# Kernel optimization log

Hardware: AMD Instinct MI355X
Metric: run time of the kernel (lower is better)

## Reference

```python
import jax, jax.numpy as jnp
import numpy as np

DOWNSAMPLE = 1  # downsample_factor


def _grid(out_h, out_w):
    # rows: x in [-1,1] along width, y in [-1,1] along height, ones
    x_t = jnp.linspace(-1.0, 1.0, out_w, dtype=jnp.float32)
    y_t = jnp.linspace(-1.0, 1.0, out_h, dtype=jnp.float32)
    xg = jnp.tile(x_t[None, :], (out_h, 1)).reshape(-1)
    yg = jnp.tile(y_t[:, None], (1, out_w)).reshape(-1)
    return jnp.stack([xg, yg, jnp.ones_like(xg)], axis=0)  # [3, P]


def spatial_transform(X, theta):
    B, C, H, W = X.shape
    out_h, out_w = H // DOWNSAMPLE, W // DOWNSAMPLE
    grid = _grid(out_h, out_w)                               # [3, P]
    Tg = jnp.einsum('bij,jp->bip', theta.reshape(B, 2, 3), grid)  # [B,2,P]
    x_s, y_s = Tg[:, 0], Tg[:, 1]                            # [B, P]

    # map from [-1,1] to pixel coords (same convention as original)
    x = (x_s + 1.0) * (W / 2.0)
    y = (y_s + 1.0) * (H / 2.0)
    x0 = jnp.floor(x).astype(jnp.int32)
    x1 = x0 + 1
    y0 = jnp.floor(y).astype(jnp.int32)
    y1 = y0 + 1
    x0c = jnp.clip(x0, 0, W - 1)
    x1c = jnp.clip(x1, 0, W - 1)
    y0c = jnp.clip(y0, 0, H - 1)
    y1c = jnp.clip(y1, 0, H - 1)

    im = jnp.transpose(X, (0, 2, 3, 1)).reshape(B, H * W, C)  # [B, HW, C]

    def gather(yi, xi):
        idx = yi * W + xi                                      # [B, P]
        return jnp.take_along_axis(im, idx[:, :, None], axis=1)  # [B, P, C]

    Ia = gather(y0c, x0c)
    Ib = gather(y1c, x0c)
    Ic = gather(y0c, x1c)
    Id = gather(y1c, x1c)

    x0f = x0c.astype(jnp.float32)
    x1f = x1c.astype(jnp.float32)
    y0f = y0c.astype(jnp.float32)
    y1f = y1c.astype(jnp.float32)
    wa = ((x1f - x) * (y1f - y))[:, :, None]
    wb = ((x1f - x) * (y - y0f))[:, :, None]
    wc = ((x - x0f) * (y1f - y))[:, :, None]
    wd = ((x - x0f) * (y - y0f))[:, :, None]

    out = wa * Ia + wb * Ib + wc * Ic + wd * Id               # [B, P, C]
    out = out.reshape(B, out_h, out_w, C)
    return jnp.transpose(out, (0, 3, 1, 2))                   # NCHW


def setup_inputs() -> dict:
    key = jax.random.key(0)
    kx, kt = jax.random.split(key)
    X = jax.random.normal(kx, (32, 3, 512, 512), dtype=jnp.float32)
    # theta near identity + noise for sensible transforms
    ident = jnp.array([1.0, 0.0, 0.0, 0.0, 1.0, 0.0], dtype=jnp.float32)
    theta = ident[None, :] + 0.1 * jax.random.normal(kt, (32, 6), dtype=jnp.float32)
    return {"X": X, "theta": theta}


def reference(X, theta):
    return spatial_transform(X, theta)
```

## Files before the change

### kernel.cpp

```cpp
#include <hip/hip_runtime.h>


#define ST_H 512
#define ST_W 512
#define ST_C 3

typedef float f2 __attribute__((ext_vector_type(2)));
struct __attribute__((packed, aligned(4))) f2_a4 { f2 v; };

__global__ __launch_bounds__(256) void st_bilinear_kernel(
    const float* __restrict__ X,
    const float* __restrict__ theta,
    float* __restrict__ out,
    int B, int chunk)
{
    int bid = blockIdx.x;
    bid = (bid & 7) * chunk + (bid >> 3);

    const int gid = bid * 256 + threadIdx.x;
    const int pix = gid & (ST_H * ST_W - 1);
    const int b   = gid >> 18;
    if (b >= B) return;

    const int h = pix >> 9;
    const int w = pix & 511;

    const float* t = theta + b * 6;
    const float t00 = t[0], t01 = t[1], t02 = t[2];
    const float t10 = t[3], t11 = t[4], t12 = t[5];

    const float xg = (float)(-1.0 + (2.0 / 511.0) * (double)w);
    const float yg = (float)(-1.0 + (2.0 / 511.0) * (double)h);

    const float x_s = t00 * xg + t01 * yg + t02;
    const float y_s = t10 * xg + t11 * yg + t12;
    const float x = (x_s + 1.0f) * (0.5f * ST_W);
    const float y = (y_s + 1.0f) * (0.5f * ST_H);

    const int x0 = (int)floorf(x);
    const int y0 = (int)floorf(y);
    const int x1 = x0 + 1, y1 = y0 + 1;

    const int x0c = min(max(x0, 0), ST_W - 1);
    const int x1c = min(max(x1, 0), ST_W - 1);
    const int y0c = min(max(y0, 0), ST_H - 1);
    const int y1c = min(max(y1, 0), ST_H - 1);

    const float x0f = (float)x0c, x1f = (float)x1c;
    const float y0f = (float)y0c, y1f = (float)y1c;
    const float wa = (x1f - x) * (y1f - y);
    const float wb = (x1f - x) * (y - y0f);
    const float wc = (x - x0f) * (y1f - y);
    const float wd = (x - x0f) * (y - y0f);

    const int xa = min(max(x0, 0), ST_W - 2);
    const bool hi = (x0 >= ST_W - 1);
    const bool lo = (x0 < 0);

    const int ia = y0c * ST_W + xa;
    const int ib = y1c * ST_W + xa;

    const float* __restrict__ Xb = X + (size_t)b * (ST_C * ST_H * ST_W);
    float* __restrict__ ob = out + (size_t)b * (ST_C * ST_H * ST_W) + pix;

#pragma unroll
    for (int c = 0; c < ST_C; ++c) {
        const float* __restrict__ Xc = Xb + c * (ST_H * ST_W);
        const f2 v0 = ((const f2_a4*)(Xc + ia))->v;
        const f2 v1 = ((const f2_a4*)(Xc + ib))->v;
        const float Ia = hi ? v0.y : v0.x;
        const float Ic = lo ? v0.x : v0.y;
        const float Ib = hi ? v1.y : v1.x;
        const float Id = lo ? v1.x : v1.y;
        const float v = wa * Ia + wb * Ib + wc * Ic + wd * Id;
        __builtin_nontemporal_store(v, ob + c * (ST_H * ST_W));
    }
}

extern "C" void kernel_launch(void* const* d_in, const int* in_sizes, int n_in,
                              void* d_out, int out_size, void* d_ws, size_t ws_size,
                              hipStream_t stream) {
    const float* X     = (const float*)d_in[0];
    const float* theta = (const float*)d_in[1];
    float* out         = (float*)d_out;

    const int B = in_sizes[1] / 6;
    const int total = B * ST_H * ST_W;
    const int block = 256;
    const int grid = (total + block - 1) / block;
    const int chunk = grid / 8;

    st_bilinear_kernel<<<grid, block, 0, stream>>>(X, theta, out, B, chunk);
}
```

Before: 47.45 us.

## Compute two adjacent output pixels per thread sharing one four-wide gather

```diff
diff --git a/kernel.cpp b/kernel.cpp
--- a/kernel.cpp
+++ b/kernel.cpp
@@ -4,9 +4,25 @@
 #define ST_H 512
 #define ST_W 512
 #define ST_C 3
+#define ST_HW (ST_H * ST_W)
 
 typedef float f2 __attribute__((ext_vector_type(2)));
+typedef float f4 __attribute__((ext_vector_type(4)));
 struct __attribute__((packed, aligned(4))) f2_a4 { f2 v; };
+struct __attribute__((packed, aligned(4))) f4_a4 { f4 v; };
+
+__device__ __forceinline__ float pick3(f4 v, int o) {
+    float r = v.x;
+    r = (o == 1) ? v.y : r;
+    r = (o == 2) ? v.z : r;
+    return r;
+}
+__device__ __forceinline__ float pick3h(f4 v, int o) {
+    float r = v.y;
+    r = (o == 1) ? v.z : r;
+    r = (o == 2) ? v.w : r;
+    return r;
+}
 
 __global__ __launch_bounds__(256) void st_bilinear_kernel(
     const float* __restrict__ X,
@@ -17,64 +33,95 @@
     int bid = blockIdx.x;
     bid = (bid & 7) * chunk + (bid >> 3);
 
-    const int gid = bid * 256 + threadIdx.x;
-    const int pix = gid & (ST_H * ST_W - 1);
-    const int b   = gid >> 18;
-    if (b >= B) return;
-
-    const int h = pix >> 9;
-    const int w = pix & 511;
+    const int h  = bid & (ST_H - 1);
+    const int b  = bid >> 9;
+    const int w0 = (int)threadIdx.x * 2;
 
     const float* t = theta + b * 6;
     const float t00 = t[0], t01 = t[1], t02 = t[2];
     const float t10 = t[3], t11 = t[4], t12 = t[5];
 
-    const float xg = (float)(-1.0 + (2.0 / 511.0) * (double)w);
-    const float yg = (float)(-1.0 + (2.0 / 511.0) * (double)h);
+    const float STEP = (float)(2.0 / 511.0);
+    const float yg = fmaf((float)h, STEP, -1.0f);
+    const float cx = fmaf(t01, yg, t02);
+    const float cy = fmaf(t11, yg, t12);
 
-    const float x_s = t00 * xg + t01 * yg + t02;
-    const float y_s = t10 * xg + t11 * yg + t12;
-    const float x = (x_s + 1.0f) * (0.5f * ST_W);
-    const float y = (y_s + 1.0f) * (0.5f * ST_H);
+    float wa[2], wbm[2], wcm[2], wdm[2];
+    int xa[2], ta[2], tb[2];
+    bool hi[2], lo[2];
 
-    const int x0 = (int)floorf(x);
-    const int y0 = (int)floorf(y);
-    const int x1 = x0 + 1, y1 = y0 + 1;
+#pragma unroll
+    for (int j = 0; j < 2; ++j) {
+        const float xg = fmaf((float)(w0 + j), STEP, -1.0f);
+        const float x = (fmaf(t00, xg, cx) + 1.0f) * 256.0f;
+        const float y = (fmaf(t10, xg, cy) + 1.0f) * 256.0f;
+        const int x0 = (int)floorf(x);
+        const int y0 = (int)floorf(y);
+        const int x0c = min(max(x0, 0), ST_W - 1);
+        const int x1c = min(max(x0 + 1, 0), ST_W - 1);
+        const int y0c = min(max(y0, 0), ST_H - 1);
+        const int y1c = min(max(y0 + 1, 0), ST_H - 1);
+        const float x0f = (float)x0c, x1f = (float)x1c;
+        const float y0f = (float)y0c, y1f = (float)y1c;
+        wa[j]  = (x1f - x) * (y1f - y);
+        wbm[j] = (x1f - x) * (y - y0f);
+        wcm[j] = (x - x0f) * (y1f - y);
+        wdm[j] = (x - x0f) * (y - y0f);
+        xa[j] = min(max(x0, 0), ST_W - 2);
+        ta[j] = y0c;
+        tb[j] = y1c;
+        hi[j] = (x0 >= ST_W - 1);
+        lo[j] = (x0 < 0);
+    }
 
-    const int x0c = min(max(x0, 0), ST_W - 1);
-    const int x1c = min(max(x1, 0), ST_W - 1);
-    const int y0c = min(max(y0, 0), ST_H - 1);
-    const int y1c = min(max(y1, 0), ST_H - 1);
+    const int  base = min(xa[0], ST_W - 4);
+    const bool g0 = (xa[0] <= ST_W - 4);
+    const int  o1 = xa[1] - base;
+    const bool g1 = ((unsigned)o1 <= 2u) && (ta[1] == ta[0]) && (tb[1] == tb[0]);
 
-    const float x0f = (float)x0c, x1f = (float)x1c;
-    const float y0f = (float)y0c, y1f = (float)y1c;
-    const float wa = (x1f - x) * (y1f - y);
-    const float wb = (x1f - x) * (y - y0f);
-    const float wc = (x - x0f) * (y1f - y);
-    const float wd = (x - x0f) * (y - y0f);
-
-    const int xa = min(max(x0, 0), ST_W - 2);
-    const bool hi = (x0 >= ST_W - 1);
-    const bool lo = (x0 < 0);
-
-    const int ia = y0c * ST_W + xa;
-    const int ib = y1c * ST_W + xa;
-
-    const float* __restrict__ Xb = X + (size_t)b * (ST_C * ST_H * ST_W);
-    float* __restrict__ ob = out + (size_t)b * (ST_C * ST_H * ST_W) + pix;
+    const float* __restrict__ Xb = X + (size_t)b * (ST_C * ST_HW);
+    float* __restrict__ ob = out + (size_t)b * (ST_C * ST_HW) + h * ST_W + w0;
 
 #pragma unroll
     for (int c = 0; c < ST_C; ++c) {
-        const float* __restrict__ Xc = Xb + c * (ST_H * ST_W);
-        const f2 v0 = ((const f2_a4*)(Xc + ia))->v;
-        const f2 v1 = ((const f2_a4*)(Xc + ib))->v;
-        const float Ia = hi ? v0.y : v0.x;
-        const float Ic = lo ? v0.x : v0.y;
-        const float Ib = hi ? v1.y : v1.x;
-        const float Id = lo ? v1.x : v1.y;
-        const float v = wa * Ia + wb * Ib + wc * Ic + wd * Id;
-        __builtin_nontemporal_store(v, ob + c * (ST_H * ST_W));
+        const float* __restrict__ Xc = Xb + c * ST_HW;
+        const f4 va = ((const f4_a4*)(Xc + ta[0] * ST_W + base))->v;
+        const f4 vb = ((const f4_a4*)(Xc + tb[0] * ST_W + base))->v;
+
+        float pA0, pC0, pB0, pD0;
+        if (g0) {
+            pA0 = va.x; pC0 = va.y; pB0 = vb.x; pD0 = vb.y;
+        } else {
+            const f2 p = ((const f2_a4*)(Xc + ta[0] * ST_W + xa[0]))->v;
+            const f2 q = ((const f2_a4*)(Xc + tb[0] * ST_W + xa[0]))->v;
+            pA0 = p.x; pC0 = p.y; pB0 = q.x; pD0 = q.y;
+        }
+
+        float pA1, pC1, pB1, pD1;
+        if (g1) {
+            pA1 = pick3 (va, o1); pC1 = pick3h(va, o1);
+            pB1 = pick3 (vb, o1); pD1 = pick3h(vb, o1);
+        } else {
+            const f2 p = ((const f2_a4*)(Xc + ta[1] * ST_W + xa[1]))->v;
+            const f2 q = ((const f2_a4*)(Xc + tb[1] * ST_W + xa[1]))->v;
+            pA1 = p.x; pC1 = p.y; pB1 = q.x; pD1 = q.y;
+        }
+
+        const float Ia0 = hi[0] ? pC0 : pA0;
+        const float Ic0 = lo[0] ? pA0 : pC0;
+        const float Ib0 = hi[0] ? pD0 : pB0;
+        const float Id0 = lo[0] ? pB0 : pD0;
+        const float Ia1 = hi[1] ? pC1 : pA1;
+        const float Ic1 = lo[1] ? pA1 : pC1;
+        const float Ib1 = hi[1] ? pD1 : pB1;
+        const float Id1 = lo[1] ? pB1 : pD1;
+
+        f2 v;
+        v.x = wa[0] * Ia0 + wbm[0] * Ib0 + wcm[0] * Ic0 + wdm[0] * Id0;
+        v.y = wa[1] * Ia1 + wbm[1] * Ib1 + wcm[1] * Ic1 + wdm[1] * Id1;
+        __builtin_nontemporal_store(v, (f2*)(ob + c * ST_HW));
     }
+    (void)B;
 }
 
 extern "C" void kernel_launch(void* const* d_in, const int* in_sizes, int n_in,
@@ -85,9 +132,8 @@
     float* out         = (float*)d_out;
 
     const int B = in_sizes[1] / 6;
-    const int total = B * ST_H * ST_W;
     const int block = 256;
-    const int grid = (total + block - 1) / block;
+    const int grid = B * ST_H;
     const int chunk = grid / 8;
 
     st_bilinear_kernel<<<grid, block, 0, stream>>>(X, theta, out, B, chunk);
```

After: 49.45 us. 1.04x slower.

## Stage source footprint per 32x32 output tile in LDS for bilinear sampling

Applied to the files above, without the earlier changes.

```diff
diff --git a/kernel.cpp b/kernel.cpp
--- a/kernel.cpp
+++ b/kernel.cpp
@@ -4,76 +4,154 @@
 #define ST_H 512
 #define ST_W 512
 #define ST_C 3
+#define ST_HW (ST_H * ST_W)
+#define TILE 32
+#define RMAX 48
+#define CPITCH 49
 
 typedef float f2 __attribute__((ext_vector_type(2)));
+typedef float f4 __attribute__((ext_vector_type(4)));
 struct __attribute__((packed, aligned(4))) f2_a4 { f2 v; };
 
-__global__ __launch_bounds__(256) void st_bilinear_kernel(
+__global__ __launch_bounds__(256) void st_bilinear_tiled(
     const float* __restrict__ X,
     const float* __restrict__ theta,
     float* __restrict__ out,
-    int B, int chunk)
+    int chunk)
 {
+    __shared__ float sb[ST_C][RMAX][CPITCH];
+
     int bid = blockIdx.x;
     bid = (bid & 7) * chunk + (bid >> 3);
 
-    const int gid = bid * 256 + threadIdx.x;
-    const int pix = gid & (ST_H * ST_W - 1);
-    const int b   = gid >> 18;
-    if (b >= B) return;
-
-    const int h = pix >> 9;
-    const int w = pix & 511;
+    const int b    = bid >> 8;
+    const int tile = bid & 255;
+    const int h0 = (tile >> 4) << 5;
+    const int w0 = (tile & 15) << 5;
 
     const float* t = theta + b * 6;
     const float t00 = t[0], t01 = t[1], t02 = t[2];
     const float t10 = t[3], t11 = t[4], t12 = t[5];
+    const float STEP = (float)(2.0 / 511.0);
 
-    const float xg = (float)(-1.0 + (2.0 / 511.0) * (double)w);
-    const float yg = (float)(-1.0 + (2.0 / 511.0) * (double)h);
+    float xminf = 1e30f, xmaxf = -1e30f, yminf = 1e30f, ymaxf = -1e30f;
+    {
+        const float xs0 = fmaf((float)w0, STEP, -1.0f);
+        const float xs1 = fmaf((float)(w0 + TILE - 1), STEP, -1.0f);
+        const float ys0 = fmaf((float)h0, STEP, -1.0f);
+        const float ys1 = fmaf((float)(h0 + TILE - 1), STEP, -1.0f);
+        const float xsv[2] = { xs0, xs1 };
+        const float ysv[2] = { ys0, ys1 };
+#pragma unroll
+        for (int i = 0; i < 2; ++i)
+#pragma unroll
+            for (int j = 0; j < 2; ++j) {
+                const float cxc = fmaf(t01, ysv[j], t02);
+                const float cyc = fmaf(t11, ysv[j], t12);
+                const float xx = (fmaf(t00, xsv[i], cxc) + 1.0f) * 256.0f;
+                const float yy = (fmaf(t10, xsv[i], cyc) + 1.0f) * 256.0f;
+                xminf = fminf(xminf, xx); xmaxf = fmaxf(xmaxf, xx);
+                yminf = fminf(yminf, yy); ymaxf = fmaxf(ymaxf, yy);
+            }
+    }
+    const int xlo = (int)floorf(xminf) - 1;
+    const int ylo = (int)floorf(yminf) - 1;
+    const int RX  = (int)floorf(xmaxf) + 2 - xlo + 1;
+    const int RY  = (int)floorf(ymaxf) + 2 - ylo + 1;
 
-    const float x_s = t00 * xg + t01 * yg + t02;
-    const float y_s = t10 * xg + t11 * yg + t12;
-    const float x = (x_s + 1.0f) * (0.5f * ST_W);
-    const float y = (y_s + 1.0f) * (0.5f * ST_H);
+    const int tid  = threadIdx.x;
+    const int trow = tid >> 3;
+    const int tcol = (tid & 7) << 2;
+    const int h = h0 + trow;
 
-    const int x0 = (int)floorf(x);
-    const int y0 = (int)floorf(y);
-    const int x1 = x0 + 1, y1 = y0 + 1;
+    const float yg = fmaf((float)h, STEP, -1.0f);
+    const float cx = fmaf(t01, yg, t02);
+    const float cy = fmaf(t11, yg, t12);
 
-    const int x0c = min(max(x0, 0), ST_W - 1);
-    const int x1c = min(max(x1, 0), ST_W - 1);
-    const int y0c = min(max(y0, 0), ST_H - 1);
-    const int y1c = min(max(y1, 0), ST_H - 1);
+    const float* __restrict__ Xb = X + (size_t)b * (ST_C * ST_HW);
+    float* __restrict__ ob = out + (size_t)b * (ST_C * ST_HW) + h * ST_W + (w0 + tcol);
 
-    const float x0f = (float)x0c, x1f = (float)x1c;
-    const float y0f = (float)y0c, y1f = (float)y1c;
-    const float wa = (x1f - x) * (y1f - y);
-    const float wb = (x1f - x) * (y - y0f);
-    const float wc = (x - x0f) * (y1f - y);
-    const float wd = (x - x0f) * (y - y0f);
+    float acc[ST_C][4];
 
-    const int xa = min(max(x0, 0), ST_W - 2);
-    const bool hi = (x0 >= ST_W - 1);
-    const bool lo = (x0 < 0);
+    if (RX <= CPITCH && RY <= RMAX) {
+        const int lane = tid & 63, wid = tid >> 6;
+        const int colc = min(max(xlo + lane, 0), ST_W - 1);
+#pragma unroll
+        for (int c = 0; c < ST_C; ++c) {
+            const float* __restrict__ Xc = Xb + c * ST_HW;
+            for (int r = wid; r < RY; r += 4) {
+                const int rowc = min(max(ylo + r, 0), ST_H - 1);
+                if (lane < CPITCH)
+                    sb[c][r][lane] = Xc[rowc * ST_W + colc];
+            }
+        }
+        __syncthreads();
 
-    const int ia = y0c * ST_W + xa;
-    const int ib = y1c * ST_W + xa;
+#pragma unroll
+        for (int j = 0; j < 4; ++j) {
+            const float xg = fmaf((float)(w0 + tcol + j), STEP, -1.0f);
+            const float x = (fmaf(t00, xg, cx) + 1.0f) * 256.0f;
+            const float y = (fmaf(t10, xg, cy) + 1.0f) * 256.0f;
+            const int x0 = (int)floorf(x);
+            const int y0 = (int)floorf(y);
+            const int x0c = min(max(x0, 0), ST_W - 1);
+            const int x1c = min(max(x0 + 1, 0), ST_W - 1);
+            const int y0c = min(max(y0, 0), ST_H - 1);
+            const int y1c = min(max(y0 + 1, 0), ST_H - 1);
+            const float wa = ((float)x1c - x) * ((float)y1c - y);
+            const float wb = ((float)x1c - x) * (y - (float)y0c);
+            const float wc = (x - (float)x0c) * ((float)y1c - y);
+            const float wd = (x - (float)x0c) * (y - (float)y0c);
+            const int lx = x0 - xlo;
+            const int ly = y0 - ylo;
+#pragma unroll
+            for (int c = 0; c < ST_C; ++c) {
+                const f2 p = ((const f2_a4*)&sb[c][ly][lx])->v;
+                const f2 q = ((const f2_a4*)&sb[c][ly + 1][lx])->v;
+                acc[c][j] = wa * p.x + wb * q.x + wc * p.y + wd * q.y;
+            }
+        }
+    } else {
+#pragma unroll
+        for (int j = 0; j < 4; ++j) {
+            const float xg = fmaf((float)(w0 + tcol + j), STEP, -1.0f);
+            const float x = (fmaf(t00, xg, cx) + 1.0f) * 256.0f;
+            const float y = (fmaf(t10, xg, cy) + 1.0f) * 256.0f;
+            const int x0 = (int)floorf(x);
+            const int y0 = (int)floorf(y);
+            const int x0c = min(max(x0, 0), ST_W - 1);
+            const int x1c = min(max(x0 + 1, 0), ST_W - 1);
+            const int y0c = min(max(y0, 0), ST_H - 1);
+            const int y1c = min(max(y0 + 1, 0), ST_H - 1);
+            const float wa = ((float)x1c - x) * ((float)y1c - y);
+            const float wb = ((float)x1c - x) * (y - (float)y0c);
+            const float wc = (x - (float)x0c) * ((float)y1c - y);
+            const float wd = (x - (float)x0c) * (y - (float)y0c);
 
-    const float* __restrict__ Xb = X + (size_t)b * (ST_C * ST_H * ST_W);
-    float* __restrict__ ob = out + (size_t)b * (ST_C * ST_H * ST_W) + pix;
+            const int xa = min(max(x0, 0), ST_W - 2);
+            const bool hi = (x0 >= ST_W - 1);
+            const bool lo = (x0 < 0);
+            const int ia = y0c * ST_W + xa;
+            const int ib = y1c * ST_W + xa;
+#pragma unroll
+            for (int c = 0; c < ST_C; ++c) {
+                const float* __restrict__ Xc = Xb + c * ST_HW;
+                const f2 p = ((const f2_a4*)(Xc + ia))->v;
+                const f2 q = ((const f2_a4*)(Xc + ib))->v;
+                const float Ia = hi ? p.y : p.x;
+                const float Ic = lo ? p.x : p.y;
+                const float Ib = hi ? q.y : q.x;
+                const float Id = lo ? q.x : q.y;
+                acc[c][j] = wa * Ia + wb * Ib + wc * Ic + wd * Id;
+            }
+        }
+    }
 
 #pragma unroll
     for (int c = 0; c < ST_C; ++c) {
-        const float* __restrict__ Xc = Xb + c * (ST_H * ST_W);
-        const f2 v0 = ((const f2_a4*)(Xc + ia))->v;
-        const f2 v1 = ((const f2_a4*)(Xc + ib))->v;
-        const float Ia = hi ? v0.y : v0.x;
-        const float Ic = lo ? v0.x : v0.y;
-        const float Ib = hi ? v1.y : v1.x;
-        const float Id = lo ? v1.x : v1.y;
-        const float v = wa * Ia + wb * Ib + wc * Ic + wd * Id;
-        __builtin_nontemporal_store(v, ob + c * (ST_H * ST_W));
+        f4 v;
+        v.x = acc[c][0]; v.y = acc[c][1]; v.z = acc[c][2]; v.w = acc[c][3];
+        __builtin_nontemporal_store(v, (f4*)(ob + c * ST_HW));
     }
 }
 
@@ -85,10 +163,9 @@
     float* out         = (float*)d_out;
 
     const int B = in_sizes[1] / 6;
-    const int total = B * ST_H * ST_W;
     const int block = 256;
-    const int grid = (total + block - 1) / block;
+    const int grid = B * 256;
     const int chunk = grid / 8;
 
-    st_bilinear_kernel<<<grid, block, 0, stream>>>(X, theta, out, B, chunk);
+    st_bilinear_tiled<<<grid, block, 0, stream>>>(X, theta, out, chunk);
 }
```

Measured after the change: 80.22 us. +69.1%, slower.
